# Kernel optimization log

Measured on AMD Instinct MI355X. Metric: run time of the kernel, lower is better.

## Reference

```python
import jax, jax.numpy as jnp
import numpy as np

BN_EPS = 1e-5


def setup_inputs() -> dict:
    key = jax.random.key(0)
    ks = jax.random.split(key, 9)
    N, C, T, V, S, INTER, OUT = 64, 64, 300, 25, 3, 16, 64
    return {
        "x": jax.random.normal(ks[0], (N, C, T, V), dtype=jnp.float32),
        "A": jax.random.uniform(ks[1], (S, V, V), dtype=jnp.float32),
        "PA": jax.random.normal(ks[2], (S, V, V), dtype=jnp.float32) * 1e-3,
        "Wa": jax.random.normal(ks[3], (S, INTER, C), dtype=jnp.float32) * 0.1,
        "ba": jax.random.normal(ks[4], (S, INTER), dtype=jnp.float32) * 0.1,
        "Wb": jax.random.normal(ks[5], (S, INTER, C), dtype=jnp.float32) * 0.1,
        "bb": jax.random.normal(ks[6], (S, INTER), dtype=jnp.float32) * 0.1,
        "Wd": jax.random.normal(ks[7], (S, OUT, C), dtype=jnp.float32) * 0.1,
        "bd": jax.random.normal(ks[8], (S, OUT), dtype=jnp.float32) * 0.1,
        "gamma": jnp.ones((OUT,), dtype=jnp.float32),
        "beta": jnp.zeros((OUT,), dtype=jnp.float32),
    }


def reference(x, A, PA, Wa, ba, Wb, bb, Wd, bd, gamma, beta):
    N, C, T, V = x.shape
    S, INTER = Wa.shape[0], Wa.shape[1]
    K = INTER * T  # contraction length for attention

    # 1x1 convs for all subsets at once: [N,S,inter,T,V]
    fa = jnp.einsum('nctv,sic->nsitv', x, Wa) + ba[None, :, :, None, None]
    fb = jnp.einsum('nctv,sic->nsitv', x, Wb) + bb[None, :, :, None, None]

    # A1: permute(0,3,1,2).view(N,V,inter*T)  -> [N,S,V,K]
    A1 = fa.transpose(0, 1, 4, 2, 3).reshape(N, S, V, K)
    # A2: view(N,inter*T,V)                   -> [N,S,K,V]
    A2 = fb.reshape(N, S, K, V)

    # attention: softmax over dim=-2, plus learned adjacency
    att = jnp.einsum('nsvk,nskw->nsvw', A1, A2) / jnp.asarray(K, x.dtype)
    att = jax.nn.softmax(att, axis=-2) + (A + PA)[None]  # [N,S,V,V]

    # message passing: x.view(N,C*T,V) @ att, then 1x1 conv_d, summed over subsets
    xm = jnp.einsum('nkv,nsvw->nskw', x.reshape(N, C * T, V), att)
    xm = xm.reshape(N, S, C, T, V)
    y = jnp.einsum('nsctv,soc->notv', xm, Wd) + bd.sum(0)[None, :, None, None]

    # BatchNorm2d (training-mode batch stats, per-channel over N,T,V)
    mean = y.mean(axis=(0, 2, 3), keepdims=True)
    var = y.var(axis=(0, 2, 3), keepdims=True)
    y = gamma[None, :, None, None] * (y - mean) * jax.lax.rsqrt(var + BN_EPS) \
        + beta[None, :, None, None]

    # residual (in_channels == out_channels -> identity down) + relu
    return jax.nn.relu(y + x)
```

## Files before the change

### kernel.cpp

```cpp
#include <hip/hip_runtime.h>
#include <math.h>

constexpr int Nn = 64, Cc = 64, Tt = 300, Vv = 25, Ss = 3, Ii = 16, Oo = 64;
constexpr int TVc  = Tt * Vv;
constexpr int CTVc = Cc * TVc;
constexpr float KINV = 1.0f / 4800.0f;

constexpr int WS_ATT  = 0;
constexpr int WS_SUM  = 120000;
constexpr int WS_SQ   = 120064;
constexpr int WS_MEAN = 120128;
constexpr int WS_RSTD = 120192;
constexpr int WS_ZERO_FLOATS = 120128;
constexpr int WS_XB_F = 120256;
constexpr size_t XB_BYTES = (size_t)Nn * TVc * Cc * 2;
constexpr size_t WS_NEED  = (size_t)WS_XB_F * 4 + XB_BYTES;

typedef __attribute__((ext_vector_type(8))) short bf16x8;
typedef __attribute__((ext_vector_type(4))) short short4v;
typedef __attribute__((ext_vector_type(4))) float f32x4;
typedef __attribute__((ext_vector_type(16))) float f32x16;
typedef __attribute__((ext_vector_type(4))) int int4v;

__device__ __forceinline__ short f2bf(float f) {
    unsigned u = __builtin_bit_cast(unsigned, f);
    u += 0x7FFFu + ((u >> 16) & 1u);
    return (short)(u >> 16);
}
__device__ __forceinline__ float bf2f(short s) {
    unsigned u = ((unsigned)(unsigned short)s) << 16;
    return __builtin_bit_cast(float, u);
}
__device__ __forceinline__ void store4(float* p, f32x4 v) {
    __builtin_memcpy(p, &v, 16);
}

__global__ __launch_bounds__(256) void k0_xpose(
    const float* __restrict__ x, short* __restrict__ xb)
{
    const int n   = blockIdx.y;
    const int tid = threadIdx.x;
    const int tv  = blockIdx.x * 32 + (tid & 31);
    const int g   = (tid >> 5) & 7;
    if (tv >= TVc) return;
    const float* xp = x + (size_t)n * CTVc + (size_t)(g * 8) * TVc + tv;
    bf16x8 o;
    #pragma unroll
    for (int j = 0; j < 8; ++j) o[j] = f2bf(xp[(size_t)j * TVc]);
    *(bf16x8*)(xb + ((size_t)n * TVc + tv) * 64 + g * 8) = o;
}

template<bool XB>
__device__ __forceinline__ void load_xfrag(
    const float* __restrict__ xn, const short* __restrict__ xbn,
    int tv, bool ok, int quad, bf16x8& b0, bf16x8& b1)
{
    if constexpr (XB) {
        const short* bp = xbn + (ok ? tv : 0) * 64 + quad * 8;
        b0 = *(const bf16x8*)bp;
        b1 = *(const bf16x8*)(bp + 32);
    } else {
        const float* bp = xn + (quad * 8) * TVc + tv;
        #pragma unroll
        for (int j = 0; j < 8; ++j) {
            b0[j] = f2bf(ok ? bp[j * TVc] : 0.0f);
            b1[j] = f2bf(ok ? bp[(j + 32) * TVc] : 0.0f);
        }
    }
}

template<bool XB>
__global__ __launch_bounds__(256) void ka_gram_mfma(
    const float* __restrict__ x, const short* __restrict__ xb,
    const float* __restrict__ Wa, const float* __restrict__ ba,
    const float* __restrict__ Wb, const float* __restrict__ bb,
    float* __restrict__ att)
{
    __shared__ short uT[112 * 104];
    __shared__ float part[4 * 1024];
    __shared__ float bab[96];

    const int tid = threadIdx.x;
    const int t0  = blockIdx.x * 4;
    const int n   = blockIdx.y;
    const float* xn  = x + n * CTVc + t0 * 25;
    const short* xbn = XB ? (xb + ((size_t)n * TVc + t0 * 25) * 64) : nullptr;

    if (tid < 96) {
        const int s = tid >> 5, r = tid & 31;
        bab[tid] = (r < 16) ? ba[s * 16 + r] : bb[s * 16 + r - 16];
    }

    const int lane = tid & 63;
    const int wave = tid >> 6;
    const int l16  = lane & 15;
    const int quad = lane >> 4;

    bf16x8 afr[3][2][2];
    #pragma unroll
    for (int s = 0; s < 3; ++s)
        #pragma unroll
        for (int half = 0; half < 2; ++half)
            #pragma unroll
            for (int k = 0; k < 2; ++k) {
                const float* W = half ? Wb : Wa;
                const float* wp = W + (s * 16 + l16) * 64 + k * 32 + quad * 8;
                const float4 w0 = *(const float4*)wp;
                const float4 w1 = *(const float4*)(wp + 4);
                bf16x8 a;
                a[0] = f2bf(w0.x); a[1] = f2bf(w0.y); a[2] = f2bf(w0.z); a[3] = f2bf(w0.w);
                a[4] = f2bf(w1.x); a[5] = f2bf(w1.y); a[6] = f2bf(w1.z); a[7] = f2bf(w1.w);
                afr[s][half][k] = a;
            }
    __syncthreads();

    for (int nt = wave; nt < 7; nt += 4) {
        const int tv = nt * 16 + l16;
        const bool ok = tv < 100;
        bf16x8 b0, b1;
        load_xfrag<XB>(xn, xbn, tv, ok, quad, b0, b1);
        #pragma unroll
        for (int s = 0; s < 3; ++s)
            #pragma unroll
            for (int half = 0; half < 2; ++half) {
                f32x4 acc = {0.0f, 0.0f, 0.0f, 0.0f};
                acc = __builtin_amdgcn_mfma_f32_16x16x32_bf16(afr[s][half][0], b0, acc, 0, 0, 0);
                acc = __builtin_amdgcn_mfma_f32_16x16x32_bf16(afr[s][half][1], b1, acc, 0, 0, 0);
                const float4 bv = *(const float4*)(bab + s * 32 + half * 16 + quad * 4);
                short4v pk;
                pk[0] = f2bf(acc[0] + bv.x); pk[1] = f2bf(acc[1] + bv.y);
                pk[2] = f2bf(acc[2] + bv.z); pk[3] = f2bf(acc[3] + bv.w);
                *(short4v*)(uT + tv * 104 + s * 32 + half * 16 + quad * 4) = pk;
            }
    }
    __syncthreads();

    const int t   = wave;
    const int w32 = lane & 31;
    const int khi = lane >> 5;
    f32x16 g[3];
    #pragma unroll
    for (int s = 0; s < 3; ++s)
        #pragma unroll
        for (int r = 0; r < 16; ++r) g[s][r] = 0.0f;

    #pragma unroll
    for (int s = 0; s < 3; ++s) {
        const short* base = uT + (t * 25 + w32) * 104 + s * 32 + khi * 8;
        const bf16x8 aA = *(const bf16x8*)(base);
        const bf16x8 bB = *(const bf16x8*)(base + 16);
        g[s] = __builtin_amdgcn_mfma_f32_32x32x16_bf16(aA, bB, g[s], 0, 0, 0);
    }

    for (int s = 0; s < 3; ++s) {
        __syncthreads();
        #pragma unroll
        for (int r = 0; r < 16; ++r) {
            const int row = (r & 3) + 8 * (r >> 2) + 4 * khi;
            part[wave * 1024 + row * 32 + w32] = g[s][r];
        }
        __syncthreads();
        float* attns = att + (n * 3 + s) * 625;
        for (int p = tid; p < 625; p += 256) {
            const int v = p / 25, w = p - v * 25;
            const int q = v * 32 + w;
            atomicAdd(attns + p, part[q] + part[1024 + q] + part[2048 + q] + part[3072 + q]);
        }
    }
}

__global__ __launch_bounds__(64) void kb_softmax(
    float* __restrict__ att, const float* __restrict__ A, const float* __restrict__ PA)
{
    const int b = blockIdx.x;
    const int s = b % 3;
    const int w = threadIdx.x;
    if (w >= 25) return;
    float* base = att + b * 625;
    float col[25];
    float m = -1e30f;
    #pragma unroll
    for (int v = 0; v < 25; ++v) {
        col[v] = base[v * 25 + w] * KINV;
        m = fmaxf(m, col[v]);
    }
    float sum = 0.0f;
    #pragma unroll
    for (int v = 0; v < 25; ++v) { col[v] = expf(col[v] - m); sum += col[v]; }
    const float inv = 1.0f / sum;
    #pragma unroll
    for (int v = 0; v < 25; ++v)
        base[v * 25 + w] = fmaf(col[v], inv, A[(s * 25 + v) * 25 + w] + PA[(s * 25 + v) * 25 + w]);
}

template<bool XB>
__global__ __launch_bounds__(256) void k3_y_mfma(
    const float* __restrict__ x, const short* __restrict__ xb,
    const float* __restrict__ Wd,
    const float* __restrict__ att, float* __restrict__ y, float* __restrict__ bns)
{
    __shared__ __align__(16) short U[96 * 128];
    __shared__ __align__(16) short attT[3 * 1024];
    __shared__ float bn1[4][32], bn2[4][32];

    const int tid = threadIdx.x;
    const int t0  = blockIdx.x * 4;
    const int n   = blockIdx.y;
    const int oh  = blockIdx.z;
    const float* xn  = x + n * CTVc + t0 * 25;
    const short* xbn = XB ? (xb + ((size_t)n * TVc + t0 * 25) * 64) : nullptr;

    const int lane = tid & 63;
    const int wave = tid >> 6;
    const int l16  = lane & 15;
    const int quad = lane >> 4;

    for (int i = tid; i < 1536; i += 256)
        ((int4v*)U)[i] = (int4v){0, 0, 0, 0};

    for (int i = tid; i < 3072; i += 256) {
        const int s = i >> 10, r = i & 1023, v = r >> 5, vp = r & 31;
        const float val = (v < 25 && vp < 25) ? att[(n * 3 + s) * 625 + vp * 25 + v] : 0.0f;
        attT[i] = f2bf(val);
    }

    bf16x8 afr[3][2][2];
    #pragma unroll
    for (int s = 0; s < 3; ++s)
        #pragma unroll
        for (int m = 0; m < 2; ++m)
            #pragma unroll
            for (int k = 0; k < 2; ++k) {
                const float* wp = Wd + ((s * 64 + oh * 32 + m * 16 + l16) * 64) + k * 32 + quad * 8;
                const float4 w0 = *(const float4*)wp;
                const float4 w1 = *(const float4*)(wp + 4);
                bf16x8 a;
                a[0] = f2bf(w0.x); a[1] = f2bf(w0.y); a[2] = f2bf(w0.z); a[3] = f2bf(w0.w);
                a[4] = f2bf(w1.x); a[5] = f2bf(w1.y); a[6] = f2bf(w1.z); a[7] = f2bf(w1.w);
                afr[s][m][k] = a;
            }
    __syncthreads();

    for (int nt = wave; nt < 7; nt += 4) {
        const int tv = nt * 16 + l16;
        const bool ok = tv < 100;
        bf16x8 b0, b1;
        load_xfrag<XB>(xn, xbn, tv, ok, quad, b0, b1);
        const int tl  = tv / 25;
        const int vp  = tv - tl * 25;
        const int col = tl * 32 + vp;
        const int grp = col >> 3, ing = col & 7;
        #pragma unroll
        for (int s = 0; s < 3; ++s)
            #pragma unroll
            for (int m = 0; m < 2; ++m) {
                f32x4 acc = {0.0f, 0.0f, 0.0f, 0.0f};
                acc = __builtin_amdgcn_mfma_f32_16x16x32_bf16(afr[s][m][0], b0, acc, 0, 0, 0);
                acc = __builtin_amdgcn_mfma_f32_16x16x32_bf16(afr[s][m][1], b1, acc, 0, 0, 0);
                if (ok) {
                    #pragma unroll
                    for (int r = 0; r < 4; ++r) {
                        const int row = s * 32 + m * 16 + quad * 4 + r;
                        U[row * 128 + (((grp ^ (row & 15)) << 3) | ing)] = f2bf(acc[r]);
                    }
                }
            }
    }
    __syncthreads();

    const int t = wave;
    bf16x8 aF[3][2], bF[3][2];
    #pragma unroll
    for (int s = 0; s < 3; ++s) {
        #pragma unroll
        for (int mt = 0; mt < 2; ++mt)
            aF[s][mt] = *(const bf16x8*)(attT + s * 1024 + (mt * 16 + l16) * 32 + quad * 8);
        #pragma unroll
        for (int nb = 0; nb < 2; ++nb) {
            const int row = s * 32 + nb * 16 + l16;
            bF[s][nb] = *(const bf16x8*)(U + row * 128 + (((t * 4 + quad) ^ (row & 15)) << 3));
        }
    }
    f32x4 D[2][2];
    #pragma unroll
    for (int mt = 0; mt < 2; ++mt)
        #pragma unroll
        for (int nb = 0; nb < 2; ++nb) D[mt][nb] = (f32x4){0.0f, 0.0f, 0.0f, 0.0f};
    #pragma unroll
    for (int s = 0; s < 3; ++s)
        #pragma unroll
        for (int mt = 0; mt < 2; ++mt)
            #pragma unroll
            for (int nb = 0; nb < 2; ++nb)
                D[mt][nb] = __builtin_amdgcn_mfma_f32_16x16x32_bf16(aF[s][mt], bF[s][nb], D[mt][nb], 0, 0, 0);

    float s1[2] = {0.0f, 0.0f}, s2[2] = {0.0f, 0.0f};
    #pragma unroll
    for (int nb = 0; nb < 2; ++nb) {
        const int og = oh * 32 + nb * 16 + l16;
        float* dst = y + ((size_t)(n * 64 + og) * 300 + t0 + t) * 25;
        const f32x4 d0 = D[0][nb];
        store4(dst + quad * 4, d0);
        s1[nb] += d0[0] + d0[1] + d0[2] + d0[3];
        s2[nb] += d0[0]*d0[0] + d0[1]*d0[1] + d0[2]*d0[2] + d0[3]*d0[3];
        const f32x4 d1 = D[1][nb];
        if (quad < 2) {
            store4(dst + 16 + quad * 4, d1);
            s1[nb] += d1[0] + d1[1] + d1[2] + d1[3];
            s2[nb] += d1[0]*d1[0] + d1[1]*d1[1] + d1[2]*d1[2] + d1[3]*d1[3];
        } else if (quad == 2) {
            dst[24] = d1[0];
            s1[nb] += d1[0];
            s2[nb] += d1[0] * d1[0];
        }
    }
    #pragma unroll
    for (int nb = 0; nb < 2; ++nb) {
        s1[nb] += __shfl_xor(s1[nb], 16); s1[nb] += __shfl_xor(s1[nb], 32);
        s2[nb] += __shfl_xor(s2[nb], 16); s2[nb] += __shfl_xor(s2[nb], 32);
    }
    if (lane < 16) {
        bn1[wave][lane]      = s1[0];
        bn1[wave][16 + lane] = s1[1];
        bn2[wave][lane]      = s2[0];
        bn2[wave][16 + lane] = s2[1];
    }
    __syncthreads();
    if (tid < 32) {
        const float S1 = bn1[0][tid] + bn1[1][tid] + bn1[2][tid] + bn1[3][tid];
        const float S2 = bn2[0][tid] + bn2[1][tid] + bn2[2][tid] + bn2[3][tid];
        atomicAdd(bns + oh * 32 + tid, S1);
        atomicAdd(bns + 64 + oh * 32 + tid, S2);
    }
}

__global__ __launch_bounds__(64) void k3b_stats(float* __restrict__ ws)
{
    const int o = threadIdx.x;
    if (o >= 64) return;
    const float cnt_inv = 1.0f / 480000.0f;
    const float s = ws[WS_SUM + o], q = ws[WS_SQ + o];
    const float mean = s * cnt_inv;
    const float var  = q * cnt_inv - mean * mean;
    ws[WS_MEAN + o] = mean;
    ws[WS_RSTD + o] = rsqrtf(var + 1e-5f);
}

__global__ __launch_bounds__(256) void k4_bn(
    float* __restrict__ out, const float* __restrict__ x,
    const float* __restrict__ gamma, const float* __restrict__ beta,
    const float* __restrict__ ws)
{
    const int i4 = blockIdx.x * 256 + threadIdx.x;
    const int o = (i4 / 1875) & 63;
    const float mean = ws[WS_MEAN + o], rstd = ws[WS_RSTD + o];
    const float g = gamma[o], b = beta[o];
    const float4 yv = ((const float4*)out)[i4];
    const float4 xv = ((const float4*)x)[i4];
    float4 r;
    r.x = fmaxf(fmaf(g * (yv.x - mean), rstd, b) + xv.x, 0.0f);
    r.y = fmaxf(fmaf(g * (yv.y - mean), rstd, b) + xv.y, 0.0f);
    r.z = fmaxf(fmaf(g * (yv.z - mean), rstd, b) + xv.z, 0.0f);
    r.w = fmaxf(fmaf(g * (yv.w - mean), rstd, b) + xv.w, 0.0f);
    ((float4*)out)[i4] = r;
}

extern "C" void kernel_launch(void* const* d_in, const int* in_sizes, int n_in,
                              void* d_out, int out_size, void* d_ws, size_t ws_size,
                              hipStream_t stream)
{
    const float* x  = (const float*)d_in[0];
    const float* A  = (const float*)d_in[1];
    const float* PA = (const float*)d_in[2];
    const float* Wa = (const float*)d_in[3];
    const float* ba = (const float*)d_in[4];
    const float* Wb = (const float*)d_in[5];
    const float* bb = (const float*)d_in[6];
    const float* Wd = (const float*)d_in[7];
    const float* gamma = (const float*)d_in[9];
    const float* beta  = (const float*)d_in[10];
    float* out = (float*)d_out;
    float* ws  = (float*)d_ws;

    hipMemsetAsync(d_ws, 0, (size_t)WS_ZERO_FLOATS * sizeof(float), stream);

    if (ws_size >= WS_NEED) {
        short* xb = (short*)(ws + WS_XB_F);
        k0_xpose<<<dim3(235, 64), 256, 0, stream>>>(x, xb);
        ka_gram_mfma<true><<<dim3(75, 64), 256, 0, stream>>>(x, xb, Wa, ba, Wb, bb, ws + WS_ATT);
        kb_softmax<<<dim3(192), 64, 0, stream>>>(ws + WS_ATT, A, PA);
        k3_y_mfma<true><<<dim3(75, 64, 2), 256, 0, stream>>>(x, xb, Wd, ws + WS_ATT, out, ws + WS_SUM);
    } else {
        ka_gram_mfma<false><<<dim3(75, 64), 256, 0, stream>>>(x, nullptr, Wa, ba, Wb, bb, ws + WS_ATT);
        kb_softmax<<<dim3(192), 64, 0, stream>>>(ws + WS_ATT, A, PA);
        k3_y_mfma<false><<<dim3(75, 64, 2), 256, 0, stream>>>(x, nullptr, Wd, ws + WS_ATT, out, ws + WS_SUM);
    }
    k3b_stats<<<dim3(1), 64, 0, stream>>>(ws);
    k4_bn<<<dim3(30000), 256, 0, stream>>>(out, x, gamma, beta, ws);
}
```

Measured before the change: 560.5 us.

## Prepack bf16 weights and attention, merge output halves in y kernel

Adds a small kernel that converts Wa/Wb/Wd to bf16 once, and has the softmax kernel emit a padded, transposed bf16 attention tile. The y kernel now runs 512 threads covering all 64 output channels per block instead of two z-halves, which avoids recomputing the Wd·x projection and reloading x twice. BN stat atomics are spread over 8 partial slots to reduce contention, and the BN kernel uses a 3D grid so the channel index needs no division. The cost is an extra launch and larger LDS per block.

```diff
diff --git a/kernel.cpp b/kernel.cpp
--- a/kernel.cpp
+++ b/kernel.cpp
@@ -8,13 +8,16 @@
 
 constexpr int WS_ATT  = 0;
 constexpr int WS_SUM  = 120000;
-constexpr int WS_SQ   = 120064;
-constexpr int WS_MEAN = 120128;
-constexpr int WS_RSTD = 120192;
-constexpr int WS_ZERO_FLOATS = 120128;
-constexpr int WS_XB_F = 120256;
-constexpr size_t XB_BYTES = (size_t)Nn * TVc * Cc * 2;
-constexpr size_t WS_NEED  = (size_t)WS_XB_F * 4 + XB_BYTES;
+constexpr int WS_SQ   = 120512;
+constexpr int WS_MEAN = 121024;
+constexpr int WS_RSTD = 121088;
+constexpr int WS_ZERO_FLOATS = 121024;
+constexpr int WS_XB_F   = 121152;
+constexpr int WS_WAB_F  = WS_XB_F + 15360000;
+constexpr int WS_WDB_F  = WS_WAB_F + 3072;
+constexpr int WS_ATTB_F = WS_WDB_F + 6144;
+constexpr int WS_END_F  = WS_ATTB_F + 98304;
+constexpr size_t WS_NEED = (size_t)WS_END_F * 4;
 
 typedef __attribute__((ext_vector_type(8))) short bf16x8;
 typedef __attribute__((ext_vector_type(4))) short short4v;
@@ -50,6 +53,20 @@
     *(bf16x8*)(xb + ((size_t)n * TVc + tv) * 64 + g * 8) = o;
 }
 
+__global__ __launch_bounds__(256) void kpack(
+    const float* __restrict__ Wa, const float* __restrict__ Wb,
+    const float* __restrict__ Wd, short* __restrict__ wab, short* __restrict__ wdb)
+{
+    const int i = blockIdx.x * 256 + threadIdx.x;
+    if (i < 6144) {
+        const int s = i >> 11, rb = i & 2047, r = rb >> 6, c = rb & 63;
+        const float v = (r < 16) ? Wa[(s * 16 + r) * 64 + c]
+                                 : Wb[(s * 16 + (r - 16)) * 64 + c];
+        wab[i] = f2bf(v);
+    }
+    if (i < 12288) wdb[i] = f2bf(Wd[i]);
+}
+
 template<bool XB>
 __device__ __forceinline__ void load_xfrag(
     const float* __restrict__ xn, const short* __restrict__ xbn,
@@ -72,6 +89,7 @@
 template<bool XB>
 __global__ __launch_bounds__(256) void ka_gram_mfma(
     const float* __restrict__ x, const short* __restrict__ xb,
+    const short* __restrict__ wab,
     const float* __restrict__ Wa, const float* __restrict__ ba,
     const float* __restrict__ Wb, const float* __restrict__ bb,
     float* __restrict__ att)
@@ -103,14 +121,19 @@
         for (int half = 0; half < 2; ++half)
             #pragma unroll
             for (int k = 0; k < 2; ++k) {
-                const float* W = half ? Wb : Wa;
-                const float* wp = W + (s * 16 + l16) * 64 + k * 32 + quad * 8;
-                const float4 w0 = *(const float4*)wp;
-                const float4 w1 = *(const float4*)(wp + 4);
-                bf16x8 a;
-                a[0] = f2bf(w0.x); a[1] = f2bf(w0.y); a[2] = f2bf(w0.z); a[3] = f2bf(w0.w);
-                a[4] = f2bf(w1.x); a[5] = f2bf(w1.y); a[6] = f2bf(w1.z); a[7] = f2bf(w1.w);
-                afr[s][half][k] = a;
+                if constexpr (XB) {
+                    afr[s][half][k] = *(const bf16x8*)(
+                        wab + (s * 32 + half * 16 + l16) * 64 + k * 32 + quad * 8);
+                } else {
+                    const float* W = half ? Wb : Wa;
+                    const float* wp = W + (s * 16 + l16) * 64 + k * 32 + quad * 8;
+                    const float4 w0 = *(const float4*)wp;
+                    const float4 w1 = *(const float4*)(wp + 4);
+                    bf16x8 a;
+                    a[0] = f2bf(w0.x); a[1] = f2bf(w0.y); a[2] = f2bf(w0.z); a[3] = f2bf(w0.w);
+                    a[4] = f2bf(w1.x); a[5] = f2bf(w1.y); a[6] = f2bf(w1.z); a[7] = f2bf(w1.w);
+                    afr[s][half][k] = a;
+                }
             }
     __syncthreads();
 
@@ -169,34 +192,161 @@
     }
 }
 
+template<bool ATTB>
 __global__ __launch_bounds__(64) void kb_softmax(
-    float* __restrict__ att, const float* __restrict__ A, const float* __restrict__ PA)
+    float* __restrict__ att, const float* __restrict__ A, const float* __restrict__ PA,
+    short* __restrict__ attb)
 {
     const int b = blockIdx.x;
     const int s = b % 3;
     const int w = threadIdx.x;
-    if (w >= 25) return;
-    float* base = att + b * 625;
-    float col[25];
-    float m = -1e30f;
-    #pragma unroll
-    for (int v = 0; v < 25; ++v) {
-        col[v] = base[v * 25 + w] * KINV;
-        m = fmaxf(m, col[v]);
-    }
-    float sum = 0.0f;
-    #pragma unroll
-    for (int v = 0; v < 25; ++v) { col[v] = expf(col[v] - m); sum += col[v]; }
-    const float inv = 1.0f / sum;
-    #pragma unroll
-    for (int v = 0; v < 25; ++v)
-        base[v * 25 + w] = fmaf(col[v], inv, A[(s * 25 + v) * 25 + w] + PA[(s * 25 + v) * 25 + w]);
-}
-
-template<bool XB>
-__global__ __launch_bounds__(256) void k3_y_mfma(
-    const float* __restrict__ x, const short* __restrict__ xb,
-    const float* __restrict__ Wd,
+    if (w >= 32) return;
+    float col[25] = {};
+    if (w < 25) {
+        float* base = att + b * 625;
+        float m = -1e30f;
+        #pragma unroll
+        for (int v = 0; v < 25; ++v) {
+            col[v] = base[v * 25 + w] * KINV;
+            m = fmaxf(m, col[v]);
+        }
+        float sum = 0.0f;
+        #pragma unroll
+        for (int v = 0; v < 25; ++v) { col[v] = expf(col[v] - m); sum += col[v]; }
+        const float inv = 1.0f / sum;
+        #pragma unroll
+        for (int v = 0; v < 25; ++v) {
+            col[v] = fmaf(col[v], inv, A[(s * 25 + v) * 25 + w] + PA[(s * 25 + v) * 25 + w]);
+            base[v * 25 + w] = col[v];
+        }
+    }
+    if constexpr (ATTB) {
+        short* dst = attb + b * 1024 + w * 32;
+        #pragma unroll
+        for (int v = 0; v < 25; ++v) dst[v] = (w < 25) ? f2bf(col[v]) : (short)0;
+        #pragma unroll
+        for (int v = 25; v < 32; ++v) dst[v] = 0;
+    }
+}
+
+__global__ __launch_bounds__(512, 4) void k3_y_mfma(
+    const short* __restrict__ xb, const short* __restrict__ wdb,
+    const short* __restrict__ attb, float* __restrict__ y, float* __restrict__ bns)
+{
+    __shared__ __align__(16) short U[192 * 128];
+    __shared__ float bnA[8][32], bnB[8][32];
+
+    const int tid = threadIdx.x;
+    const int t0  = blockIdx.x * 4;
+    const int n   = blockIdx.y;
+    const short* xbn = xb + ((size_t)n * TVc + t0 * 25) * 64;
+
+    const int lane = tid & 63;
+    const int wave = tid >> 6;
+    const int l16  = lane & 15;
+    const int quad = lane >> 4;
+
+    for (int i = tid; i < 3072; i += 512)
+        ((int4v*)U)[i] = (int4v){0, 0, 0, 0};
+    __syncthreads();
+
+    if (wave < 7) {
+        const int tv = wave * 16 + l16;
+        const bool ok = tv < 100;
+        const short* bp = xbn + (ok ? tv : 0) * 64 + quad * 8;
+        const bf16x8 b0 = *(const bf16x8*)bp;
+        const bf16x8 b1 = *(const bf16x8*)(bp + 32);
+        const int tl  = tv / 25;
+        const int vp  = tv - tl * 25;
+        const int col = tl * 32 + vp;
+        const int grp = col >> 3, ing = col & 7;
+        #pragma unroll
+        for (int s = 0; s < 3; ++s)
+            #pragma unroll
+            for (int m = 0; m < 4; ++m) {
+                const short* wp = wdb + (s * 64 + m * 16 + l16) * 64 + quad * 8;
+                const bf16x8 f0 = *(const bf16x8*)wp;
+                const bf16x8 f1 = *(const bf16x8*)(wp + 32);
+                f32x4 acc = {0.0f, 0.0f, 0.0f, 0.0f};
+                acc = __builtin_amdgcn_mfma_f32_16x16x32_bf16(f0, b0, acc, 0, 0, 0);
+                acc = __builtin_amdgcn_mfma_f32_16x16x32_bf16(f1, b1, acc, 0, 0, 0);
+                if (ok) {
+                    #pragma unroll
+                    for (int r = 0; r < 4; ++r) {
+                        const int row = s * 64 + m * 16 + quad * 4 + r;
+                        U[row * 128 + (((grp ^ (row & 15)) << 3) | ing)] = f2bf(acc[r]);
+                    }
+                }
+            }
+    }
+    __syncthreads();
+
+    const int t  = wave >> 1;
+    const int ob = (wave & 1) * 32;
+    f32x4 D[2][2];
+    #pragma unroll
+    for (int mt = 0; mt < 2; ++mt)
+        #pragma unroll
+        for (int nb = 0; nb < 2; ++nb) D[mt][nb] = (f32x4){0.0f, 0.0f, 0.0f, 0.0f};
+    #pragma unroll
+    for (int s = 0; s < 3; ++s) {
+        const short* ab = attb + (size_t)(n * 3 + s) * 1024 + l16 * 32 + quad * 8;
+        const bf16x8 a0 = *(const bf16x8*)ab;
+        const bf16x8 a1 = *(const bf16x8*)(ab + 512);
+        #pragma unroll
+        for (int nb = 0; nb < 2; ++nb) {
+            const int row = s * 64 + ob + nb * 16 + l16;
+            const bf16x8 bv = *(const bf16x8*)(
+                U + row * 128 + (((t * 4 + quad) ^ (row & 15)) << 3));
+            D[0][nb] = __builtin_amdgcn_mfma_f32_16x16x32_bf16(a0, bv, D[0][nb], 0, 0, 0);
+            D[1][nb] = __builtin_amdgcn_mfma_f32_16x16x32_bf16(a1, bv, D[1][nb], 0, 0, 0);
+        }
+    }
+
+    float s1[2] = {0.0f, 0.0f}, s2[2] = {0.0f, 0.0f};
+    #pragma unroll
+    for (int nb = 0; nb < 2; ++nb) {
+        const int og = ob + nb * 16 + l16;
+        float* dst = y + ((size_t)(n * 64 + og) * 300 + t0 + t) * 25;
+        const f32x4 d0 = D[0][nb];
+        store4(dst + quad * 4, d0);
+        s1[nb] += d0[0] + d0[1] + d0[2] + d0[3];
+        s2[nb] += d0[0]*d0[0] + d0[1]*d0[1] + d0[2]*d0[2] + d0[3]*d0[3];
+        const f32x4 d1 = D[1][nb];
+        if (quad < 2) {
+            store4(dst + 16 + quad * 4, d1);
+            s1[nb] += d1[0] + d1[1] + d1[2] + d1[3];
+            s2[nb] += d1[0]*d1[0] + d1[1]*d1[1] + d1[2]*d1[2] + d1[3]*d1[3];
+        } else if (quad == 2) {
+            dst[24] = d1[0];
+            s1[nb] += d1[0];
+            s2[nb] += d1[0] * d1[0];
+        }
+    }
+    #pragma unroll
+    for (int nb = 0; nb < 2; ++nb) {
+        s1[nb] += __shfl_xor(s1[nb], 16); s1[nb] += __shfl_xor(s1[nb], 32);
+        s2[nb] += __shfl_xor(s2[nb], 16); s2[nb] += __shfl_xor(s2[nb], 32);
+    }
+    if (lane < 16) {
+        bnA[wave][lane]      = s1[0];
+        bnA[wave][16 + lane] = s1[1];
+        bnB[wave][lane]      = s2[0];
+        bnB[wave][16 + lane] = s2[1];
+    }
+    __syncthreads();
+    if (tid < 64) {
+        const int o = tid, h = o >> 5, i = o & 31;
+        const float S1 = bnA[h][i] + bnA[h + 2][i] + bnA[h + 4][i] + bnA[h + 6][i];
+        const float S2 = bnB[h][i] + bnB[h + 2][i] + bnB[h + 4][i] + bnB[h + 6][i];
+        const int cp = (blockIdx.x & 7) * 64;
+        atomicAdd(bns + cp + o, S1);
+        atomicAdd(bns + 512 + cp + o, S2);
+    }
+}
+
+__global__ __launch_bounds__(256) void k3_y_mfma_fb(
+    const float* __restrict__ x, const float* __restrict__ Wd,
     const float* __restrict__ att, float* __restrict__ y, float* __restrict__ bns)
 {
     __shared__ __align__(16) short U[96 * 128];
@@ -207,8 +357,7 @@
     const int t0  = blockIdx.x * 4;
     const int n   = blockIdx.y;
     const int oh  = blockIdx.z;
-    const float* xn  = x + n * CTVc + t0 * 25;
-    const short* xbn = XB ? (xb + ((size_t)n * TVc + t0 * 25) * 64) : nullptr;
+    const float* xn = x + n * CTVc + t0 * 25;
 
     const int lane = tid & 63;
     const int wave = tid >> 6;
@@ -217,13 +366,11 @@
 
     for (int i = tid; i < 1536; i += 256)
         ((int4v*)U)[i] = (int4v){0, 0, 0, 0};
-
     for (int i = tid; i < 3072; i += 256) {
         const int s = i >> 10, r = i & 1023, v = r >> 5, vp = r & 31;
         const float val = (v < 25 && vp < 25) ? att[(n * 3 + s) * 625 + vp * 25 + v] : 0.0f;
         attT[i] = f2bf(val);
     }
-
     bf16x8 afr[3][2][2];
     #pragma unroll
     for (int s = 0; s < 3; ++s)
@@ -245,7 +392,7 @@
         const int tv = nt * 16 + l16;
         const bool ok = tv < 100;
         bf16x8 b0, b1;
-        load_xfrag<XB>(xn, xbn, tv, ok, quad, b0, b1);
+        load_xfrag<false>(xn, nullptr, tv, ok, quad, b0, b1);
         const int tl  = tv / 25;
         const int vp  = tv - tl * 25;
         const int col = tl * 32 + vp;
@@ -329,8 +476,9 @@
     if (tid < 32) {
         const float S1 = bn1[0][tid] + bn1[1][tid] + bn1[2][tid] + bn1[3][tid];
         const float S2 = bn2[0][tid] + bn2[1][tid] + bn2[2][tid] + bn2[3][tid];
-        atomicAdd(bns + oh * 32 + tid, S1);
-        atomicAdd(bns + 64 + oh * 32 + tid, S2);
+        const int cp = (blockIdx.x & 7) * 64;
+        atomicAdd(bns + cp + oh * 32 + tid, S1);
+        atomicAdd(bns + 512 + cp + oh * 32 + tid, S2);
     }
 }
 
@@ -339,7 +487,12 @@
     const int o = threadIdx.x;
     if (o >= 64) return;
     const float cnt_inv = 1.0f / 480000.0f;
-    const float s = ws[WS_SUM + o], q = ws[WS_SQ + o];
+    float s = 0.0f, q = 0.0f;
+    #pragma unroll
+    for (int j = 0; j < 8; ++j) {
+        s += ws[WS_SUM + j * 64 + o];
+        q += ws[WS_SQ  + j * 64 + o];
+    }
     const float mean = s * cnt_inv;
     const float var  = q * cnt_inv - mean * mean;
     ws[WS_MEAN + o] = mean;
@@ -351,8 +504,10 @@
     const float* __restrict__ gamma, const float* __restrict__ beta,
     const float* __restrict__ ws)
 {
-    const int i4 = blockIdx.x * 256 + threadIdx.x;
-    const int o = (i4 / 1875) & 63;
+    const int o = blockIdx.y, n = blockIdx.z;
+    const int j = blockIdx.x * 256 + threadIdx.x;
+    if (j >= 1875) return;
+    const size_t i4 = (size_t)(n * 64 + o) * 1875 + j;
     const float mean = ws[WS_MEAN + o], rstd = ws[WS_RSTD + o];
     const float g = gamma[o], b = beta[o];
     const float4 yv = ((const float4*)out)[i4];
@@ -385,16 +540,23 @@
     hipMemsetAsync(d_ws, 0, (size_t)WS_ZERO_FLOATS * sizeof(float), stream);
 
     if (ws_size >= WS_NEED) {
-        short* xb = (short*)(ws + WS_XB_F);
-        k0_xpose<<<dim3(235, 64), 256, 0, stream>>>(x, xb);
-        ka_gram_mfma<true><<<dim3(75, 64), 256, 0, stream>>>(x, xb, Wa, ba, Wb, bb, ws + WS_ATT);
-        kb_softmax<<<dim3(192), 64, 0, stream>>>(ws + WS_ATT, A, PA);
-        k3_y_mfma<true><<<dim3(75, 64, 2), 256, 0, stream>>>(x, xb, Wd, ws + WS_ATT, out, ws + WS_SUM);
+        short* xbp  = (short*)(ws + WS_XB_F);
+        short* wab  = (short*)(ws + WS_WAB_F);
+        short* wdb  = (short*)(ws + WS_WDB_F);
+        short* attb = (short*)(ws + WS_ATTB_F);
+        k0_xpose<<<dim3(235, 64), 256, 0, stream>>>(x, xbp);
+        kpack<<<dim3(48), 256, 0, stream>>>(Wa, Wb, Wd, wab, wdb);
+        ka_gram_mfma<true><<<dim3(75, 64), 256, 0, stream>>>(
+            x, xbp, wab, Wa, ba, Wb, bb, ws + WS_ATT);
+        kb_softmax<true><<<dim3(192), 64, 0, stream>>>(ws + WS_ATT, A, PA, attb);
+        k3_y_mfma<<<dim3(75, 64), 512, 0, stream>>>(xbp, wdb, attb, out, ws + WS_SUM);
     } else {
-        ka_gram_mfma<false><<<dim3(75, 64), 256, 0, stream>>>(x, nullptr, Wa, ba, Wb, bb, ws + WS_ATT);
-        kb_softmax<<<dim3(192), 64, 0, stream>>>(ws + WS_ATT, A, PA);
-        k3_y_mfma<false><<<dim3(75, 64, 2), 256, 0, stream>>>(x, nullptr, Wd, ws + WS_ATT, out, ws + WS_SUM);
+        ka_gram_mfma<false><<<dim3(75, 64), 256, 0, stream>>>(
+            x, nullptr, nullptr, Wa, ba, Wb, bb, ws + WS_ATT);
+        kb_softmax<false><<<dim3(192), 64, 0, stream>>>(ws + WS_ATT, A, PA, nullptr);
+        k3_y_mfma_fb<<<dim3(75, 64, 2), 256, 0, stream>>>(
+            x, Wd, ws + WS_ATT, out, ws + WS_SUM);
     }
     k3b_stats<<<dim3(1), 64, 0, stream>>>(ws);
-    k4_bn<<<dim3(30000), 256, 0, stream>>>(out, x, gamma, beta, ws);
-}
+    k4_bn<<<dim3(8, 64, 64), 256, 0, stream>>>(out, x, gamma, beta, ws);
+}
```

New measurement: 484.7 us. 13.5% less time.
